# Kernel tuning notes

Hardware: AMD Instinct MI355X
Metric: run time of the kernel (lower is better)

The kernel has to match this reference:

```python
import jax, jax.numpy as jnp
import numpy as np
import math

H = 12
D_MODEL = 768
D_K = D_MODEL // H


def setup_inputs() -> dict:
    key = jax.random.key(0)
    ks = jax.random.split(key, 12)
    B, L = 128, 512
    s = 1.0 / math.sqrt(D_MODEL)
    return {
        "Q": jax.random.normal(ks[0], (B, L, D_MODEL), jnp.float32),
        "K": jax.random.normal(ks[1], (B, L, D_MODEL), jnp.float32),
        "V": jax.random.normal(ks[2], (B, L, D_MODEL), jnp.float32),
        "mask": jax.random.uniform(ks[3], (B, B), jnp.float32),
        "Wq": jax.random.normal(ks[4], (D_MODEL, D_MODEL), jnp.float32) * s,
        "bq": jnp.zeros((D_MODEL,), jnp.float32),
        "Wk": jax.random.normal(ks[5], (D_MODEL, D_MODEL), jnp.float32) * s,
        "bk": jnp.zeros((D_MODEL,), jnp.float32),
        "Wv": jax.random.normal(ks[6], (D_MODEL, D_MODEL), jnp.float32) * s,
        "bv": jnp.zeros((D_MODEL,), jnp.float32),
        "Wo": jax.random.normal(ks[7], (D_MODEL, D_MODEL), jnp.float32) * s,
        "bo": jnp.zeros((D_MODEL,), jnp.float32),
    }


def reference(Q, K, V, mask, Wq, bq, Wk, bk, Wv, bv, Wo, bo):
    nb_q = Q.shape[0]   # nbatches_q = Q.size(0) in the torch code
    nb_kv = K.shape[0]
    # Linear projections then the module's exact reshape/transpose pattern.
    q = (Q @ Wq + bq).reshape(-1, nb_q, H, D_K).swapaxes(1, 2)   # (L, h, B, d_k)
    k = (K @ Wk + bk).reshape(-1, nb_kv, H, D_K).swapaxes(1, 2)  # (L, h, B, d_k)
    v = (V @ Wv + bv).reshape(-1, nb_kv, H, D_K).swapaxes(1, 2)  # (L, h, B, d_k)
    # AttentionAgger: model_dim = d_k -> scale by sqrt(d_k)
    attn = jnp.einsum('lhbd,lhed->lhbe', q, k) / math.sqrt(D_K)  # (L, h, B, B)
    # dual softmax with additive mask bias (mask scaled by its leading dim)
    m = jax.nn.softmax(mask / mask.shape[0], axis=-1)            # (B, B), broadcasts
    attn = jax.nn.softmax(attn, axis=-1) + m
    attn = jax.nn.softmax(attn, axis=-1)
    x = jnp.einsum('lhbe,lhed->lhbd', attn, v)                   # (L, h, B, d_k)
    x = x.swapaxes(1, 2).reshape(-1, nb_q, H * D_K)              # (L, B, d_model)
    return x @ Wo + bo
```

## Files before the change

kernel.cpp:

```cpp
#include <hip/hip_runtime.h>


typedef __attribute__((ext_vector_type(8))) __bf16 bf16x8;
typedef __attribute__((ext_vector_type(4))) __bf16 bf16x4;
typedef __attribute__((ext_vector_type(4))) float f32x4;

#define DM 768
#define LOG2E 1.44269504f

__device__ __forceinline__ unsigned short f2bf(float x) {
  unsigned u = __float_as_uint(x);
  u += 0x7FFFu + ((u >> 16) & 1u);
  return (unsigned short)(u >> 16);
}

__device__ __forceinline__ void gl_lds16(const void* g, void* l) {
  __builtin_amdgcn_global_load_lds(
      (const __attribute__((address_space(1))) unsigned int*)g,
      (__attribute__((address_space(3))) unsigned int*)l, 16, 0, 0);
}

__global__ __launch_bounds__(256) void prep_w(const float* __restrict__ w0,
                                              const float* __restrict__ w1,
                                              const float* __restrict__ w2,
                                              const float* __restrict__ w3,
                                              unsigned short* __restrict__ wt) {
  __shared__ float t[32][33];
  const int op = blockIdx.z;
  const float* w = (op == 0) ? w0 : (op == 1) ? w1 : (op == 2) ? w2 : w3;
  unsigned short* o = wt + (size_t)op * DM * DM;
  const int n0 = blockIdx.x * 32, k0 = blockIdx.y * 32;
  const int tx = threadIdx.x & 31, ty = threadIdx.x >> 5;
#pragma unroll
  for (int r = 0; r < 4; ++r)
    t[r * 8 + ty][tx] = w[(size_t)(k0 + r * 8 + ty) * DM + n0 + tx];
  __syncthreads();
#pragma unroll
  for (int r = 0; r < 4; ++r)
    o[(size_t)(n0 + r * 8 + ty) * DM + k0 + tx] = f2bf(t[tx][r * 8 + ty]);
}

__global__ void prep_m(const float* __restrict__ mask, float* __restrict__ mm) {
  int row = blockIdx.x;
  int t = threadIdx.x;
  float a = mask[row * 128 + t] * (1.0f / 128.0f);
  float b = mask[row * 128 + t + 64] * (1.0f / 128.0f);
  float mx = fmaxf(a, b);
  for (int s = 1; s < 64; s <<= 1) mx = fmaxf(mx, __shfl_xor(mx, s));
  float ea = __expf(a - mx), eb = __expf(b - mx);
  float sum = ea + eb;
  for (int s = 1; s < 64; s <<= 1) sum += __shfl_xor(sum, s);
  float inv = LOG2E / sum;
  mm[row * 128 + t] = ea * inv;
  mm[row * 128 + t + 64] = eb * inv;
}

__global__ __launch_bounds__(256) void convb(const float* __restrict__ in,
                                             unsigned short* __restrict__ out, int n8) {
  int i = blockIdx.x * 256 + threadIdx.x;
  const int stride = gridDim.x * 256;
  for (; i < n8; i += stride) {
    const float4 a = ((const float4*)in)[(size_t)i * 2];
    const float4 b = ((const float4*)in)[(size_t)i * 2 + 1];
    ushort4 lo = {f2bf(a.x), f2bf(a.y), f2bf(a.z), f2bf(a.w)};
    ushort4 hi = {f2bf(b.x), f2bf(b.y), f2bf(b.z), f2bf(b.w)};
    ((ushort4*)out)[(size_t)i * 2] = lo;
    ((ushort4*)out)[(size_t)i * 2 + 1] = hi;
  }
}

__device__ __forceinline__ void stage_tile(const unsigned short* __restrict__ src,
                                           int row0, int kcol, char* slotbase, int tid) {
  const int wid = tid >> 6, lane = tid & 63;
#pragma unroll
  for (int s = 0; s < 2; ++s) {
    const int row = s * 128 + wid * 16 + (lane >> 2);
    const int slot = lane & 3;
    gl_lds16(src + (size_t)(row0 + row) * DM + kcol + ((slot ^ ((row >> 1) & 3)) * 8),
             slotbase + s * 8192 + wid * 1024);
  }
}

template <bool OUT_BF16>
__global__ __launch_bounds__(512, 2) void gemm8(const unsigned short* __restrict__ A,
                                                const unsigned short* __restrict__ Bt,
                                                const float* __restrict__ bias,
                                                void* __restrict__ Outp) {
  __shared__ char smem[131072];
  const int tid = threadIdx.x, lane = tid & 63, wid = tid >> 6;
  const int cl = lane & 15, g = lane >> 4;
  const int wm = wid >> 2, wn = wid & 3;
  const int bid = blockIdx.x;
  const int xcd = bid & 7, bi = bid >> 3;
  const int m0 = (xcd * 32 + bi / 3) * 256;
  const int n0 = (bi % 3) * 256;

  f32x4 acc[8][4] = {};

  auto aslot = [&](int t) { return (char*)smem + (t & 3) * 16384; };
  auto bslot = [&](int t) { return (char*)smem + 65536 + (t & 3) * 16384; };

  auto lda = [&](bf16x8* af, int t, int half) {
#pragma unroll
    for (int mi = 0; mi < 4; ++mi) {
      const int r = wm * 128 + (half * 4 + mi) * 16 + cl;
      af[mi] = *(const bf16x8*)(aslot(t) + r * 64 + ((g ^ ((r >> 1) & 3)) * 16));
    }
  };
  auto ldb = [&](bf16x8* bf, int t) {
#pragma unroll
    for (int ni = 0; ni < 4; ++ni) {
      const int r = wn * 64 + ni * 16 + cl;
      bf[ni] = *(const bf16x8*)(bslot(t) + r * 64 + ((g ^ ((r >> 1) & 3)) * 16));
    }
  };
  auto mfma16 = [&](bf16x8* af, bf16x8* bf, int half) {
    __builtin_amdgcn_s_setprio(1);
#pragma unroll
    for (int mi = 0; mi < 4; ++mi)
#pragma unroll
      for (int ni = 0; ni < 4; ++ni)
        acc[half * 4 + mi][ni] = __builtin_amdgcn_mfma_f32_16x16x32_bf16(
            af[mi], bf[ni], acc[half * 4 + mi][ni], 0, 0, 0);
    __builtin_amdgcn_s_setprio(0);
  };

  auto gstep = [&](int t, bool stg, int vm, bf16x8* af0, bf16x8* bfc,
                   bf16x8* af0n, bf16x8* bfn, bool last) {
    bf16x8 af1[4];
    if (stg) stage_tile(A, m0, (t + 3) * 32, aslot(t + 3), tid);
    if (vm == 6)      asm volatile("s_waitcnt vmcnt(6)" ::: "memory");
    else if (vm == 4) asm volatile("s_waitcnt vmcnt(4)" ::: "memory");
    else              asm volatile("s_waitcnt vmcnt(0)" ::: "memory");
    __builtin_amdgcn_s_barrier();
    lda(af1, t, 1);
    mfma16(af0, bfc, 0);
    if (stg) stage_tile(Bt, n0, (t + 3) * 32, bslot(t + 3), tid);
    if (!last) {
      lda(af0n, t + 1, 0);
      ldb(bfn, t + 1);
    }
    mfma16(af1, bfc, 1);
    __builtin_amdgcn_s_barrier();
  };

  stage_tile(A, m0, 0, aslot(0), tid);   stage_tile(Bt, n0, 0, bslot(0), tid);
  stage_tile(A, m0, 32, aslot(1), tid);  stage_tile(Bt, n0, 32, bslot(1), tid);
  stage_tile(A, m0, 64, aslot(2), tid);  stage_tile(Bt, n0, 64, bslot(2), tid);
  asm volatile("s_waitcnt vmcnt(8)" ::: "memory");
  __builtin_amdgcn_s_barrier();

  bf16x8 afA[4], bfA[4], afB[4], bfB[4];
  lda(afA, 0, 0);
  ldb(bfA, 0);

#pragma unroll 1
  for (int t = 0; t < 20; t += 2) {
    gstep(t, true, 6, afA, bfA, afB, bfB, false);
    gstep(t + 1, true, 6, afB, bfB, afA, bfA, false);
  }
  gstep(20, true, 6, afA, bfA, afB, bfB, false);
  gstep(21, false, 4, afB, bfB, afA, bfA, false);
  gstep(22, false, 0, afA, bfA, afB, bfB, false);
  gstep(23, false, 0, afB, bfB, afA, bfA, true);

  float bb[4];
#pragma unroll
  for (int ni = 0; ni < 4; ++ni) bb[ni] = bias[n0 + wn * 64 + ni * 16 + cl];
#pragma unroll
  for (int mi = 0; mi < 8; ++mi) {
    const int row = m0 + wm * 128 + mi * 16 + g * 4;
#pragma unroll
    for (int ni = 0; ni < 4; ++ni) {
      const int col = n0 + wn * 64 + ni * 16 + cl;
#pragma unroll
      for (int e = 0; e < 4; ++e) {
        float v = acc[mi][ni][e] + bb[ni];
        if constexpr (OUT_BF16)
          ((unsigned short*)Outp)[(size_t)(row + e) * DM + col] = f2bf(v);
        else
          ((float*)Outp)[(size_t)(row + e) * DM + col] = v;
      }
    }
  }
}

__global__ __launch_bounds__(512) void attn_k(const unsigned short* __restrict__ qp,
                                              const unsigned short* __restrict__ kp,
                                              const unsigned short* __restrict__ vp,
                                              const float* __restrict__ mm,
                                              unsigned short* __restrict__ xout) {
  __shared__ char smem[32768];
  unsigned short* vt = (unsigned short*)(smem + 16384);

  const int tid = threadIdx.x, lane = tid & 63, wid = tid >> 6;
  const int cl = lane & 15, g = lane >> 4;
  const int h = blockIdx.x, l = blockIdx.y;
  const size_t base = (size_t)l * 128 * DM + h * 64;
  const int q = wid * 16 + cl;

#pragma unroll
  for (int p = 0; p < 2; ++p) {
    const int chunk = p * 8 + wid;
    const int row = chunk * 8 + (lane >> 3);
    const int gi = (lane & 7) ^ (row & 7);
    gl_lds16(kp + base + (size_t)row * DM + gi * 8, smem + chunk * 1024);
  }
  if (tid < 256) {
    const int dc = (tid & 7) * 8;
    const int kq = tid >> 3;
    const int pg = (kq ^ ((tid & 7) << 2));
    int4 r0 = *(const int4*)&vp[base + (size_t)(kq * 4 + 0) * DM + dc];
    int4 r1 = *(const int4*)&vp[base + (size_t)(kq * 4 + 1) * DM + dc];
    int4 r2 = *(const int4*)&vp[base + (size_t)(kq * 4 + 2) * DM + dc];
    int4 r3 = *(const int4*)&vp[base + (size_t)(kq * 4 + 3) * DM + dc];
    const unsigned short* u0 = (const unsigned short*)&r0;
    const unsigned short* u1 = (const unsigned short*)&r1;
    const unsigned short* u2 = (const unsigned short*)&r2;
    const unsigned short* u3 = (const unsigned short*)&r3;
#pragma unroll
    for (int j = 0; j < 8; ++j) {
      ushort4 w = {u0[j], u1[j], u2[j], u3[j]};
      *(ushort4*)&vt[(dc + j) * 128 + pg * 4] = w;
    }
  }
  bf16x8 qf[2];
#pragma unroll
  for (int ksr = 0; ksr < 2; ++ksr)
    qf[ksr] = *(const bf16x8*)&qp[base + (size_t)q * DM + ksr * 32 + g * 8];
  __syncthreads();

  f32x4 sacc[8] = {};
  __builtin_amdgcn_s_setprio(1);
#pragma unroll
  for (int ksr = 0; ksr < 2; ++ksr) {
#pragma unroll
    for (int kf = 0; kf < 8; ++kf) {
      const int row = kf * 16 + cl;
      const int gi = (ksr * 4 + g) ^ (row & 7);
      bf16x8 kfr = *(const bf16x8*)(smem + row * 128 + gi * 16);
      sacc[kf] = __builtin_amdgcn_mfma_f32_16x16x32_bf16(kfr, qf[ksr], sacc[kf], 0, 0, 0);
    }
  }
  __builtin_amdgcn_s_setprio(0);
  __syncthreads();

  bf16x4 pk[8];
  {
    float4 mrow[8];
#pragma unroll
    for (int kf = 0; kf < 8; ++kf)
      mrow[kf] = *(const float4*)&mm[q * 128 + kf * 16 + g * 4];
    float sm = 0.f;
#pragma unroll
    for (int kf = 0; kf < 8; ++kf)
#pragma unroll
      for (int e = 0; e < 4; ++e) {
        float p = exp2f(sacc[kf][e] * (0.125f * LOG2E));
        sacc[kf][e] = p;
        sm += p;
      }
    sm += __shfl_xor(sm, 16); sm += __shfl_xor(sm, 32);
    const float inv2e = LOG2E / sm;
    float s2 = 0.f;
#pragma unroll
    for (int kf = 0; kf < 8; ++kf)
#pragma unroll
      for (int e = 0; e < 4; ++e) {
        float p = exp2f(fmaf(sacc[kf][e], inv2e, ((const float*)&mrow[kf])[e]));
        sacc[kf][e] = p;
        s2 += p;
      }
    s2 += __shfl_xor(s2, 16); s2 += __shfl_xor(s2, 32);
    const float inv2 = 1.0f / s2;
#pragma unroll
    for (int kf = 0; kf < 8; ++kf)
      pk[kf] = {(__bf16)(sacc[kf][0] * inv2), (__bf16)(sacc[kf][1] * inv2),
                (__bf16)(sacc[kf][2] * inv2), (__bf16)(sacc[kf][3] * inv2)};
  }

  f32x4 xacc[4] = {};

#pragma unroll
  for (int kf = 0; kf < 4; ++kf) {
    const int gi = (kf * 4 + g) ^ ((q & 3) << 2);
    *(bf16x4*)(smem + q * 128 + gi * 8) = pk[kf];
  }
  asm volatile("s_waitcnt lgkmcnt(0)" ::: "memory");
  __builtin_amdgcn_sched_barrier(0);
  __builtin_amdgcn_s_setprio(1);
#pragma unroll
  for (int ks2 = 0; ks2 < 2; ++ks2) {
    const int gi = (ks2 * 8 + g * 2) ^ ((q & 3) << 2);
    bf16x8 pa = *(const bf16x8*)(smem + q * 128 + gi * 8);
#pragma unroll
    for (int fc = 0; fc < 4; ++fc) {
      const int d = fc * 16 + cl;
      const int pg = (ks2 * 8 + 2 * g) ^ (((d >> 3) & 7) << 2);
      bf16x8 bv = *(const bf16x8*)&vt[d * 128 + pg * 4];
      xacc[fc] = __builtin_amdgcn_mfma_f32_16x16x32_bf16(pa, bv, xacc[fc], 0, 0, 0);
    }
  }
  __builtin_amdgcn_s_setprio(0);
  asm volatile("s_waitcnt lgkmcnt(0)" ::: "memory");
  __builtin_amdgcn_sched_barrier(0);

#pragma unroll
  for (int kf = 0; kf < 4; ++kf) {
    const int gi = (kf * 4 + g) ^ ((q & 3) << 2);
    *(bf16x4*)(smem + q * 128 + gi * 8) = pk[4 + kf];
  }
  asm volatile("s_waitcnt lgkmcnt(0)" ::: "memory");
  __builtin_amdgcn_sched_barrier(0);
  __builtin_amdgcn_s_setprio(1);
#pragma unroll
  for (int ks2 = 2; ks2 < 4; ++ks2) {
    const int gi = ((ks2 - 2) * 8 + g * 2) ^ ((q & 3) << 2);
    bf16x8 pa = *(const bf16x8*)(smem + q * 128 + gi * 8);
#pragma unroll
    for (int fc = 0; fc < 4; ++fc) {
      const int d = fc * 16 + cl;
      const int pg = (ks2 * 8 + 2 * g) ^ (((d >> 3) & 7) << 2);
      bf16x8 bv = *(const bf16x8*)&vt[d * 128 + pg * 4];
      xacc[fc] = __builtin_amdgcn_mfma_f32_16x16x32_bf16(pa, bv, xacc[fc], 0, 0, 0);
    }
  }
  __builtin_amdgcn_s_setprio(0);

#pragma unroll
  for (int fc = 0; fc < 4; ++fc)
#pragma unroll
    for (int e = 0; e < 4; ++e) {
      const int qr = wid * 16 + g * 4 + e;
      __bf16 b = (__bf16)xacc[fc][e];
      unsigned short u;
      __builtin_memcpy(&u, &b, 2);
      xout[base + (size_t)qr * DM + fc * 16 + cl] = u;
    }
}

extern "C" void kernel_launch(void* const* d_in, const int* in_sizes, int n_in,
                              void* d_out, int out_size, void* d_ws, size_t ws_size,
                              hipStream_t stream) {
  (void)in_sizes; (void)n_in; (void)out_size; (void)ws_size;
  const float* Q = (const float*)d_in[0];
  const float* K = (const float*)d_in[1];
  const float* V = (const float*)d_in[2];
  const float* mask = (const float*)d_in[3];
  const float* Wq = (const float*)d_in[4];
  const float* bq = (const float*)d_in[5];
  const float* Wk = (const float*)d_in[6];
  const float* bk = (const float*)d_in[7];
  const float* Wv = (const float*)d_in[8];
  const float* bv = (const float*)d_in[9];
  const float* Wo = (const float*)d_in[10];
  const float* bo = (const float*)d_in[11];

  const size_t NP = (size_t)65536 * DM;

  unsigned short* qp = (unsigned short*)d_out;
  unsigned short* kp = qp + NP;
  unsigned short* S1 = (unsigned short*)d_ws;
  unsigned short* S2 = S1 + NP;
  unsigned short* wt = S2 + NP;
  float* mm = (float*)(wt + (size_t)4 * DM * DM);

  prep_w<<<dim3(24, 24, 4), 256, 0, stream>>>(Wq, Wk, Wv, Wo, wt);
  prep_m<<<dim3(128), 64, 0, stream>>>(mask, mm);

  const int n8 = (int)(NP / 8);
  dim3 g8(768);

  convb<<<dim3(2048), 256, 0, stream>>>(Q, S1, n8);
  gemm8<true><<<g8, 512, 0, stream>>>(S1, wt + 0 * (size_t)DM * DM, bq, qp);
  convb<<<dim3(2048), 256, 0, stream>>>(K, S1, n8);
  gemm8<true><<<g8, 512, 0, stream>>>(S1, wt + 1 * (size_t)DM * DM, bk, kp);
  convb<<<dim3(2048), 256, 0, stream>>>(V, S2, n8);
  gemm8<true><<<g8, 512, 0, stream>>>(S2, wt + 2 * (size_t)DM * DM, bv, S1);

  attn_k<<<dim3(12, 512), 512, 0, stream>>>(qp, kp, S1, mm, S1);

  gemm8<false><<<g8, 512, 0, stream>>>(S1, wt + 3 * (size_t)DM * DM, bo, (float*)d_out);
}
```

Before: 662.7 us.

## Process four sequence tiles per attention block with double-buffered K/V prefetch

The attention kernel now loops over four consecutive L tiles per block instead of one, so the grid shrinks by a factor of four. K for the next tile goes into a second LDS buffer, while V and Q for the next tile are loaded into registers during the current tile's compute. The mask rows are loaded once per block and reused across tiles. This is meant to hide global-load latency and cut per-block setup cost, but LDS use rises to 80 KB per block, which can lower the number of resident blocks per CU.

```diff
diff --git a/kernel.cpp b/kernel.cpp
--- a/kernel.cpp
+++ b/kernel.cpp
@@ -185,158 +185,184 @@
   }
 }
 
-__global__ __launch_bounds__(512) void attn_k(const unsigned short* __restrict__ qp,
-                                              const unsigned short* __restrict__ kp,
-                                              const unsigned short* __restrict__ vp,
-                                              const float* __restrict__ mm,
-                                              unsigned short* __restrict__ xout) {
-  __shared__ char smem[32768];
-  unsigned short* vt = (unsigned short*)(smem + 16384);
+#define TPB 4
+
+__global__ __launch_bounds__(512, 4) void attn_k(const unsigned short* __restrict__ qp,
+                                                 const unsigned short* __restrict__ kp,
+                                                 const unsigned short* __restrict__ vp,
+                                                 const float* __restrict__ mm,
+                                                 unsigned short* __restrict__ xout) {
+  __shared__ char smem[81920];
+  char* psb = smem + 65536;
 
   const int tid = threadIdx.x, lane = tid & 63, wid = tid >> 6;
   const int cl = lane & 15, g = lane >> 4;
-  const int h = blockIdx.x, l = blockIdx.y;
-  const size_t base = (size_t)l * 128 * DM + h * 64;
+  const int h = blockIdx.x;
+  const int l0 = blockIdx.y * TPB;
   const int q = wid * 16 + cl;
 
-#pragma unroll
-  for (int p = 0; p < 2; ++p) {
-    const int chunk = p * 8 + wid;
-    const int row = chunk * 8 + (lane >> 3);
-    const int gi = (lane & 7) ^ (row & 7);
-    gl_lds16(kp + base + (size_t)row * DM + gi * 8, smem + chunk * 1024);
-  }
-  if (tid < 256) {
-    const int dc = (tid & 7) * 8;
-    const int kq = tid >> 3;
-    const int pg = (kq ^ ((tid & 7) << 2));
-    int4 r0 = *(const int4*)&vp[base + (size_t)(kq * 4 + 0) * DM + dc];
-    int4 r1 = *(const int4*)&vp[base + (size_t)(kq * 4 + 1) * DM + dc];
-    int4 r2 = *(const int4*)&vp[base + (size_t)(kq * 4 + 2) * DM + dc];
-    int4 r3 = *(const int4*)&vp[base + (size_t)(kq * 4 + 3) * DM + dc];
-    const unsigned short* u0 = (const unsigned short*)&r0;
-    const unsigned short* u1 = (const unsigned short*)&r1;
-    const unsigned short* u2 = (const unsigned short*)&r2;
-    const unsigned short* u3 = (const unsigned short*)&r3;
-#pragma unroll
-    for (int j = 0; j < 8; ++j) {
-      ushort4 w = {u0[j], u1[j], u2[j], u3[j]};
-      *(ushort4*)&vt[(dc + j) * 128 + pg * 4] = w;
-    }
-  }
-  bf16x8 qf[2];
-#pragma unroll
-  for (int ksr = 0; ksr < 2; ++ksr)
-    qf[ksr] = *(const bf16x8*)&qp[base + (size_t)q * DM + ksr * 32 + g * 8];
-  __syncthreads();
-
-  f32x4 sacc[8] = {};
-  __builtin_amdgcn_s_setprio(1);
-#pragma unroll
-  for (int ksr = 0; ksr < 2; ++ksr) {
-#pragma unroll
-    for (int kf = 0; kf < 8; ++kf) {
-      const int row = kf * 16 + cl;
-      const int gi = (ksr * 4 + g) ^ (row & 7);
-      bf16x8 kfr = *(const bf16x8*)(smem + row * 128 + gi * 16);
-      sacc[kf] = __builtin_amdgcn_mfma_f32_16x16x32_bf16(kfr, qf[ksr], sacc[kf], 0, 0, 0);
-    }
-  }
-  __builtin_amdgcn_s_setprio(0);
-  __syncthreads();
-
-  bf16x4 pk[8];
-  {
-    float4 mrow[8];
-#pragma unroll
-    for (int kf = 0; kf < 8; ++kf)
-      mrow[kf] = *(const float4*)&mm[q * 128 + kf * 16 + g * 4];
-    float sm = 0.f;
-#pragma unroll
-    for (int kf = 0; kf < 8; ++kf)
+  auto ksb = [&](int t) { return smem + (t & 1) * 16384; };
+  auto vtb = [&](int t) { return (unsigned short*)(smem + 32768 + (t & 1) * 16384); };
+  auto tbase = [&](int t) { return (size_t)(l0 + t) * 128 * DM + h * 64; };
+
+  const bool vw = tid < 256;
+  const int dc = (tid & 7) * 8;
+  const int kq = (tid & 255) >> 3;
+  int4 vr[4];
+
+  auto loadV = [&](size_t base) {
+    if (vw) {
+#pragma unroll
+      for (int r = 0; r < 4; ++r)
+        vr[r] = *(const int4*)&vp[base + (size_t)(kq * 4 + r) * DM + dc];
+    }
+  };
+  auto writeVT = [&](unsigned short* vt) {
+    if (vw) {
+      const int pg = kq ^ ((tid & 7) << 2);
+      const unsigned short* u0 = (const unsigned short*)&vr[0];
+      const unsigned short* u1 = (const unsigned short*)&vr[1];
+      const unsigned short* u2 = (const unsigned short*)&vr[2];
+      const unsigned short* u3 = (const unsigned short*)&vr[3];
+#pragma unroll
+      for (int j = 0; j < 8; ++j) {
+        ushort4 w = {u0[j], u1[j], u2[j], u3[j]};
+        *(ushort4*)&vt[(dc + j) * 128 + pg * 4] = w;
+      }
+    }
+  };
+  auto stageK = [&](size_t base, char* dst) {
+#pragma unroll
+    for (int p = 0; p < 2; ++p) {
+      const int chunk = p * 8 + wid;
+      const int row = chunk * 8 + (lane >> 3);
+      const int gi = (lane & 7) ^ (row & 7);
+      gl_lds16(kp + base + (size_t)row * DM + gi * 8, dst + chunk * 1024);
+    }
+  };
+  auto loadQ = [&](size_t base, bf16x8* qf) {
+#pragma unroll
+    for (int ksr = 0; ksr < 2; ++ksr)
+      qf[ksr] = *(const bf16x8*)&qp[base + (size_t)q * DM + ksr * 32 + g * 8];
+  };
+
+  float4 mrow[8];
+#pragma unroll
+  for (int kf = 0; kf < 8; ++kf)
+    mrow[kf] = *(const float4*)&mm[q * 128 + kf * 16 + g * 4];
+
+  bf16x8 qfA[2], qfB[2];
+  loadV(tbase(0));
+  loadQ(tbase(0), qfA);
+  stageK(tbase(0), ksb(0));
+  asm volatile("s_waitcnt vmcnt(0)" ::: "memory");
+  __builtin_amdgcn_sched_barrier(0);
+
+  auto iter = [&](int t, bool pf, bf16x8* qf, bf16x8* qn) {
+    writeVT(vtb(t));
+    if (pf) { loadV(tbase(t + 1)); loadQ(tbase(t + 1), qn); }
+    asm volatile("s_waitcnt lgkmcnt(0)" ::: "memory");
+    __builtin_amdgcn_sched_barrier(0);
+    __builtin_amdgcn_s_barrier();
+    if (pf) stageK(tbase(t + 1), ksb(t + 1));
+
+    f32x4 sacc[8] = {};
+    __builtin_amdgcn_s_setprio(1);
+#pragma unroll
+    for (int ksr = 0; ksr < 2; ++ksr) {
+#pragma unroll
+      for (int kf = 0; kf < 8; ++kf) {
+        const int row = kf * 16 + cl;
+        const int gi = (ksr * 4 + g) ^ (row & 7);
+        bf16x8 kfr = *(const bf16x8*)(ksb(t) + row * 128 + gi * 16);
+        sacc[kf] =
+            __builtin_amdgcn_mfma_f32_16x16x32_bf16(kfr, qf[ksr], sacc[kf], 0, 0, 0);
+      }
+    }
+    __builtin_amdgcn_s_setprio(0);
+
+    bf16x4 pk[8];
+    {
+      float sm = 0.f;
+#pragma unroll
+      for (int kf = 0; kf < 8; ++kf)
+#pragma unroll
+        for (int e = 0; e < 4; ++e) {
+          float p = exp2f(sacc[kf][e] * (0.125f * LOG2E));
+          sacc[kf][e] = p;
+          sm += p;
+        }
+      sm += __shfl_xor(sm, 16); sm += __shfl_xor(sm, 32);
+      const float inv2e = LOG2E / sm;
+      float s2 = 0.f;
+#pragma unroll
+      for (int kf = 0; kf < 8; ++kf)
+#pragma unroll
+        for (int e = 0; e < 4; ++e) {
+          float p = exp2f(fmaf(sacc[kf][e], inv2e, ((const float*)&mrow[kf])[e]));
+          sacc[kf][e] = p;
+          s2 += p;
+        }
+      s2 += __shfl_xor(s2, 16); s2 += __shfl_xor(s2, 32);
+      const float inv2 = 1.0f / s2;
+#pragma unroll
+      for (int kf = 0; kf < 8; ++kf)
+        pk[kf] = {(__bf16)(sacc[kf][0] * inv2), (__bf16)(sacc[kf][1] * inv2),
+                  (__bf16)(sacc[kf][2] * inv2), (__bf16)(sacc[kf][3] * inv2)};
+    }
+
+    f32x4 xacc[4] = {};
+    unsigned short* vt = vtb(t);
+#pragma unroll
+    for (int half = 0; half < 2; ++half) {
+#pragma unroll
+      for (int kf = 0; kf < 4; ++kf) {
+        const int gi = (kf * 4 + g) ^ ((q & 3) << 2);
+        *(bf16x4*)(psb + q * 128 + gi * 8) = pk[half * 4 + kf];
+      }
+      asm volatile("s_waitcnt lgkmcnt(0)" ::: "memory");
+      __builtin_amdgcn_sched_barrier(0);
+      __builtin_amdgcn_s_setprio(1);
+#pragma unroll
+      for (int k2 = 0; k2 < 2; ++k2) {
+        const int ks2 = half * 2 + k2;
+        const int gi = (k2 * 8 + g * 2) ^ ((q & 3) << 2);
+        bf16x8 pa = *(const bf16x8*)(psb + q * 128 + gi * 8);
+#pragma unroll
+        for (int fc = 0; fc < 4; ++fc) {
+          const int d = fc * 16 + cl;
+          const int pg = (ks2 * 8 + 2 * g) ^ (((d >> 3) & 7) << 2);
+          bf16x8 bv = *(const bf16x8*)&vt[d * 128 + pg * 4];
+          xacc[fc] = __builtin_amdgcn_mfma_f32_16x16x32_bf16(pa, bv, xacc[fc], 0, 0, 0);
+        }
+      }
+      __builtin_amdgcn_s_setprio(0);
+      if (half == 0) {
+        asm volatile("s_waitcnt lgkmcnt(0)" ::: "memory");
+        __builtin_amdgcn_sched_barrier(0);
+      }
+    }
+
+    asm volatile("s_waitcnt vmcnt(0)" ::: "memory");
+    __builtin_amdgcn_sched_barrier(0);
+
+    const size_t base = tbase(t);
+#pragma unroll
+    for (int fc = 0; fc < 4; ++fc)
 #pragma unroll
       for (int e = 0; e < 4; ++e) {
-        float p = exp2f(sacc[kf][e] * (0.125f * LOG2E));
-        sacc[kf][e] = p;
-        sm += p;
-      }
-    sm += __shfl_xor(sm, 16); sm += __shfl_xor(sm, 32);
-    const float inv2e = LOG2E / sm;
-    float s2 = 0.f;
-#pragma unroll
-    for (int kf = 0; kf < 8; ++kf)
-#pragma unroll
-      for (int e = 0; e < 4; ++e) {
-        float p = exp2f(fmaf(sacc[kf][e], inv2e, ((const float*)&mrow[kf])[e]));
-        sacc[kf][e] = p;
-        s2 += p;
-      }
-    s2 += __shfl_xor(s2, 16); s2 += __shfl_xor(s2, 32);
-    const float inv2 = 1.0f / s2;
-#pragma unroll
-    for (int kf = 0; kf < 8; ++kf)
-      pk[kf] = {(__bf16)(sacc[kf][0] * inv2), (__bf16)(sacc[kf][1] * inv2),
-                (__bf16)(sacc[kf][2] * inv2), (__bf16)(sacc[kf][3] * inv2)};
-  }
-
-  f32x4 xacc[4] = {};
-
-#pragma unroll
-  for (int kf = 0; kf < 4; ++kf) {
-    const int gi = (kf * 4 + g) ^ ((q & 3) << 2);
-    *(bf16x4*)(smem + q * 128 + gi * 8) = pk[kf];
-  }
-  asm volatile("s_waitcnt lgkmcnt(0)" ::: "memory");
-  __builtin_amdgcn_sched_barrier(0);
-  __builtin_amdgcn_s_setprio(1);
-#pragma unroll
-  for (int ks2 = 0; ks2 < 2; ++ks2) {
-    const int gi = (ks2 * 8 + g * 2) ^ ((q & 3) << 2);
-    bf16x8 pa = *(const bf16x8*)(smem + q * 128 + gi * 8);
-#pragma unroll
-    for (int fc = 0; fc < 4; ++fc) {
-      const int d = fc * 16 + cl;
-      const int pg = (ks2 * 8 + 2 * g) ^ (((d >> 3) & 7) << 2);
-      bf16x8 bv = *(const bf16x8*)&vt[d * 128 + pg * 4];
-      xacc[fc] = __builtin_amdgcn_mfma_f32_16x16x32_bf16(pa, bv, xacc[fc], 0, 0, 0);
-    }
-  }
-  __builtin_amdgcn_s_setprio(0);
-  asm volatile("s_waitcnt lgkmcnt(0)" ::: "memory");
-  __builtin_amdgcn_sched_barrier(0);
-
-#pragma unroll
-  for (int kf = 0; kf < 4; ++kf) {
-    const int gi = (kf * 4 + g) ^ ((q & 3) << 2);
-    *(bf16x4*)(smem + q * 128 + gi * 8) = pk[4 + kf];
-  }
-  asm volatile("s_waitcnt lgkmcnt(0)" ::: "memory");
-  __builtin_amdgcn_sched_barrier(0);
-  __builtin_amdgcn_s_setprio(1);
-#pragma unroll
-  for (int ks2 = 2; ks2 < 4; ++ks2) {
-    const int gi = ((ks2 - 2) * 8 + g * 2) ^ ((q & 3) << 2);
-    bf16x8 pa = *(const bf16x8*)(smem + q * 128 + gi * 8);
-#pragma unroll
-    for (int fc = 0; fc < 4; ++fc) {
-      const int d = fc * 16 + cl;
-      const int pg = (ks2 * 8 + 2 * g) ^ (((d >> 3) & 7) << 2);
-      bf16x8 bv = *(const bf16x8*)&vt[d * 128 + pg * 4];
-      xacc[fc] = __builtin_amdgcn_mfma_f32_16x16x32_bf16(pa, bv, xacc[fc], 0, 0, 0);
-    }
-  }
-  __builtin_amdgcn_s_setprio(0);
-
-#pragma unroll
-  for (int fc = 0; fc < 4; ++fc)
-#pragma unroll
-    for (int e = 0; e < 4; ++e) {
-      const int qr = wid * 16 + g * 4 + e;
-      __bf16 b = (__bf16)xacc[fc][e];
-      unsigned short u;
-      __builtin_memcpy(&u, &b, 2);
-      xout[base + (size_t)qr * DM + fc * 16 + cl] = u;
-    }
+        const int qr = wid * 16 + g * 4 + e;
+        __bf16 b = (__bf16)xacc[fc][e];
+        unsigned short u;
+        __builtin_memcpy(&u, &b, 2);
+        xout[base + (size_t)qr * DM + fc * 16 + cl] = u;
+      }
+  };
+
+  iter(0, true, qfA, qfB);
+  iter(1, true, qfB, qfA);
+  iter(2, true, qfA, qfB);
+  iter(3, false, qfB, qfA);
 }
 
 extern "C" void kernel_launch(void* const* d_in, const int* in_sizes, int n_in,
@@ -378,7 +404,7 @@
   convb<<<dim3(2048), 256, 0, stream>>>(V, S2, n8);
   gemm8<true><<<g8, 512, 0, stream>>>(S2, wt + 2 * (size_t)DM * DM, bv, S1);
 
-  attn_k<<<dim3(12, 512), 512, 0, stream>>>(qp, kp, S1, mm, S1);
+  attn_k<<<dim3(12, 128), 512, 0, stream>>>(qp, kp, S1, mm, S1);
 
   gemm8<false><<<g8, 512, 0, stream>>>(S1, wt + 3 * (size_t)DM * DM, bo, (float*)d_out);
 }
```

Measured after the change: 760.0 us. 1.15x slower.

## Fuse fp32-to-bf16 input conversion into projection GEMM A-tile loading

Applied to the files above, without the earlier changes.

Removes the separate convb kernels that converted Q, K and V to bf16 in workspace. The projection GEMM now loads fp32 A rows into registers, converts them to bf16 and writes them into the swizzled LDS slots one pipeline step ahead, with waitcnt counts adjusted to match. This drops a full read-write round trip of three large activation tensors. In exchange the GEMM reads twice as many A bytes, uses more registers for staging, and adds LDS writes plus an lgkmcnt wait inside each step. The attention PV loop is also folded into a loop over halves, which is only cosmetic.

```diff
diff --git a/kernel.cpp b/kernel.cpp
--- a/kernel.cpp
+++ b/kernel.cpp
@@ -18,6 +18,17 @@
   __builtin_amdgcn_global_load_lds(
       (const __attribute__((address_space(1))) unsigned int*)g,
       (__attribute__((address_space(3))) unsigned int*)l, 16, 0, 0);
+}
+
+__device__ __forceinline__ void waitvm(int n) {
+  switch (n) {
+    case 0:  asm volatile("s_waitcnt vmcnt(0)" ::: "memory"); break;
+    case 2:  asm volatile("s_waitcnt vmcnt(2)" ::: "memory"); break;
+    case 4:  asm volatile("s_waitcnt vmcnt(4)" ::: "memory"); break;
+    case 6:  asm volatile("s_waitcnt vmcnt(6)" ::: "memory"); break;
+    case 8:  asm volatile("s_waitcnt vmcnt(8)" ::: "memory"); break;
+    default: asm volatile("s_waitcnt vmcnt(10)" ::: "memory"); break;
+  }
 }
 
 __global__ __launch_bounds__(256) void prep_w(const float* __restrict__ w0,
@@ -55,20 +66,6 @@
   mm[row * 128 + t + 64] = eb * inv;
 }
 
-__global__ __launch_bounds__(256) void convb(const float* __restrict__ in,
-                                             unsigned short* __restrict__ out, int n8) {
-  int i = blockIdx.x * 256 + threadIdx.x;
-  const int stride = gridDim.x * 256;
-  for (; i < n8; i += stride) {
-    const float4 a = ((const float4*)in)[(size_t)i * 2];
-    const float4 b = ((const float4*)in)[(size_t)i * 2 + 1];
-    ushort4 lo = {f2bf(a.x), f2bf(a.y), f2bf(a.z), f2bf(a.w)};
-    ushort4 hi = {f2bf(b.x), f2bf(b.y), f2bf(b.z), f2bf(b.w)};
-    ((ushort4*)out)[(size_t)i * 2] = lo;
-    ((ushort4*)out)[(size_t)i * 2 + 1] = hi;
-  }
-}
-
 __device__ __forceinline__ void stage_tile(const unsigned short* __restrict__ src,
                                            int row0, int kcol, char* slotbase, int tid) {
   const int wid = tid >> 6, lane = tid & 63;
@@ -81,12 +78,14 @@
   }
 }
 
-template <bool OUT_BF16>
-__global__ __launch_bounds__(512, 2) void gemm8(const unsigned short* __restrict__ A,
+template <bool OUT_BF16, bool A_FP32>
+__global__ __launch_bounds__(512, 2) void gemm8(const void* __restrict__ Ap,
                                                 const unsigned short* __restrict__ Bt,
                                                 const float* __restrict__ bias,
                                                 void* __restrict__ Outp) {
   __shared__ char smem[131072];
+  const unsigned short* A16 = (const unsigned short*)Ap;
+  const float* A32 = (const float*)Ap;
   const int tid = threadIdx.x, lane = tid & 63, wid = tid >> 6;
   const int cl = lane & 15, g = lane >> 4;
   const int wm = wid >> 2, wn = wid & 3;
@@ -100,6 +99,28 @@
   auto aslot = [&](int t) { return (char*)smem + (t & 3) * 16384; };
   auto bslot = [&](int t) { return (char*)smem + 65536 + (t & 3) * 16384; };
 
+  const int arow = tid >> 1, ahalf = tid & 1;
+  float4 ar0[4], ar1[4];
+  auto aloadR = [&](int t, float4* buf) {
+    const float* src = &A32[(size_t)(m0 + arow) * DM + t * 32 + ahalf * 16];
+#pragma unroll
+    for (int i = 0; i < 4; ++i) buf[i] = *(const float4*)(src + i * 4);
+  };
+  auto awrite = [&](int t, const float4* buf) {
+    const float* f = (const float*)buf;
+    bf16x8 v0, v1;
+#pragma unroll
+    for (int j = 0; j < 8; ++j) {
+      v0[j] = (__bf16)f[j];
+      v1[j] = (__bf16)f[8 + j];
+    }
+    const int m = (arow >> 1) & 3;
+    const int s0 = (ahalf * 2) ^ m;
+    char* base = aslot(t) + arow * 64;
+    *(bf16x8*)(base + s0 * 16) = v0;
+    *(bf16x8*)(base + (s0 ^ 1) * 16) = v1;
+  };
+
   auto lda = [&](bf16x8* af, int t, int half) {
 #pragma unroll
     for (int mi = 0; mi < 4; ++mi) {
@@ -125,13 +146,15 @@
     __builtin_amdgcn_s_setprio(0);
   };
 
-  auto gstep = [&](int t, bool stg, int vm, bf16x8* af0, bf16x8* bfc,
-                   bf16x8* af0n, bf16x8* bfn, bool last) {
+  auto gstep = [&](int t, bool stg, int vm, bool wr, float4* arL, float4* arW,
+                   bf16x8* af0, bf16x8* bfc, bf16x8* af0n, bf16x8* bfn, bool last) {
     bf16x8 af1[4];
-    if (stg) stage_tile(A, m0, (t + 3) * 32, aslot(t + 3), tid);
-    if (vm == 6)      asm volatile("s_waitcnt vmcnt(6)" ::: "memory");
-    else if (vm == 4) asm volatile("s_waitcnt vmcnt(4)" ::: "memory");
-    else              asm volatile("s_waitcnt vmcnt(0)" ::: "memory");
+    if constexpr (A_FP32) {
+      if (stg) aloadR(t + 3, arL);
+    } else {
+      if (stg) stage_tile(A16, m0, (t + 3) * 32, aslot(t + 3), tid);
+    }
+    waitvm(vm);
     __builtin_amdgcn_s_barrier();
     lda(af1, t, 1);
     mfma16(af0, bfc, 0);
@@ -141,28 +164,59 @@
       ldb(bfn, t + 1);
     }
     mfma16(af1, bfc, 1);
+    if constexpr (A_FP32) {
+      if (wr) {
+        awrite(t + 2, arW);
+        asm volatile("s_waitcnt lgkmcnt(0)" ::: "memory");
+        __builtin_amdgcn_sched_barrier(0);
+      }
+    }
     __builtin_amdgcn_s_barrier();
   };
 
-  stage_tile(A, m0, 0, aslot(0), tid);   stage_tile(Bt, n0, 0, bslot(0), tid);
-  stage_tile(A, m0, 32, aslot(1), tid);  stage_tile(Bt, n0, 32, bslot(1), tid);
-  stage_tile(A, m0, 64, aslot(2), tid);  stage_tile(Bt, n0, 64, bslot(2), tid);
-  asm volatile("s_waitcnt vmcnt(8)" ::: "memory");
-  __builtin_amdgcn_s_barrier();
+  if constexpr (A_FP32) {
+    aloadR(0, ar0);
+    stage_tile(Bt, n0, 0, bslot(0), tid);
+    aloadR(1, ar1);
+    stage_tile(Bt, n0, 32, bslot(1), tid);
+    waitvm(8);
+    awrite(0, ar0);
+    aloadR(2, ar0);
+    waitvm(6);
+    awrite(1, ar1);
+    stage_tile(Bt, n0, 64, bslot(2), tid);
+    asm volatile("s_waitcnt lgkmcnt(0)" ::: "memory");
+    __builtin_amdgcn_sched_barrier(0);
+    __builtin_amdgcn_s_barrier();
+  } else {
+    stage_tile(A16, m0, 0, aslot(0), tid);  stage_tile(Bt, n0, 0, bslot(0), tid);
+    stage_tile(A16, m0, 32, aslot(1), tid); stage_tile(Bt, n0, 32, bslot(1), tid);
+    stage_tile(A16, m0, 64, aslot(2), tid); stage_tile(Bt, n0, 64, bslot(2), tid);
+    asm volatile("s_waitcnt vmcnt(8)" ::: "memory");
+    __builtin_amdgcn_s_barrier();
+  }
 
   bf16x8 afA[4], bfA[4], afB[4], bfB[4];
   lda(afA, 0, 0);
   ldb(bfA, 0);
 
+  constexpr int VMs = A_FP32 ? 10 : 6;
 #pragma unroll 1
   for (int t = 0; t < 20; t += 2) {
-    gstep(t, true, 6, afA, bfA, afB, bfB, false);
-    gstep(t + 1, true, 6, afB, bfB, afA, bfA, false);
-  }
-  gstep(20, true, 6, afA, bfA, afB, bfB, false);
-  gstep(21, false, 4, afB, bfB, afA, bfA, false);
-  gstep(22, false, 0, afA, bfA, afB, bfB, false);
-  gstep(23, false, 0, afB, bfB, afA, bfA, true);
+    gstep(t, true, VMs, true, ar1, ar0, afA, bfA, afB, bfB, false);
+    gstep(t + 1, true, VMs, true, ar0, ar1, afB, bfB, afA, bfA, false);
+  }
+  if constexpr (A_FP32) {
+    gstep(20, true, 10, true, ar1, ar0, afA, bfA, afB, bfB, false);
+    gstep(21, false, 6, true, ar0, ar1, afB, bfB, afA, bfA, false);
+    gstep(22, false, 0, false, ar1, ar0, afA, bfA, afB, bfB, false);
+    gstep(23, false, 0, false, ar0, ar1, afB, bfB, afA, bfA, true);
+  } else {
+    gstep(20, true, 6, false, ar1, ar0, afA, bfA, afB, bfB, false);
+    gstep(21, false, 4, false, ar0, ar1, afB, bfB, afA, bfA, false);
+    gstep(22, false, 0, false, ar1, ar0, afA, bfA, afB, bfB, false);
+    gstep(23, false, 0, false, ar0, ar1, afB, bfB, afA, bfA, true);
+  }
 
   float bb[4];
 #pragma unroll
@@ -280,52 +334,35 @@
   }
 
   f32x4 xacc[4] = {};
-
-#pragma unroll
-  for (int kf = 0; kf < 4; ++kf) {
-    const int gi = (kf * 4 + g) ^ ((q & 3) << 2);
-    *(bf16x4*)(smem + q * 128 + gi * 8) = pk[kf];
-  }
-  asm volatile("s_waitcnt lgkmcnt(0)" ::: "memory");
-  __builtin_amdgcn_sched_barrier(0);
-  __builtin_amdgcn_s_setprio(1);
-#pragma unroll
-  for (int ks2 = 0; ks2 < 2; ++ks2) {
-    const int gi = (ks2 * 8 + g * 2) ^ ((q & 3) << 2);
-    bf16x8 pa = *(const bf16x8*)(smem + q * 128 + gi * 8);
-#pragma unroll
-    for (int fc = 0; fc < 4; ++fc) {
-      const int d = fc * 16 + cl;
-      const int pg = (ks2 * 8 + 2 * g) ^ (((d >> 3) & 7) << 2);
-      bf16x8 bv = *(const bf16x8*)&vt[d * 128 + pg * 4];
-      xacc[fc] = __builtin_amdgcn_mfma_f32_16x16x32_bf16(pa, bv, xacc[fc], 0, 0, 0);
-    }
-  }
-  __builtin_amdgcn_s_setprio(0);
-  asm volatile("s_waitcnt lgkmcnt(0)" ::: "memory");
-  __builtin_amdgcn_sched_barrier(0);
-
-#pragma unroll
-  for (int kf = 0; kf < 4; ++kf) {
-    const int gi = (kf * 4 + g) ^ ((q & 3) << 2);
-    *(bf16x4*)(smem + q * 128 + gi * 8) = pk[4 + kf];
-  }
-  asm volatile("s_waitcnt lgkmcnt(0)" ::: "memory");
-  __builtin_amdgcn_sched_barrier(0);
-  __builtin_amdgcn_s_setprio(1);
-#pragma unroll
-  for (int ks2 = 2; ks2 < 4; ++ks2) {
-    const int gi = ((ks2 - 2) * 8 + g * 2) ^ ((q & 3) << 2);
-    bf16x8 pa = *(const bf16x8*)(smem + q * 128 + gi * 8);
-#pragma unroll
-    for (int fc = 0; fc < 4; ++fc) {
-      const int d = fc * 16 + cl;
-      const int pg = (ks2 * 8 + 2 * g) ^ (((d >> 3) & 7) << 2);
-      bf16x8 bv = *(const bf16x8*)&vt[d * 128 + pg * 4];
-      xacc[fc] = __builtin_amdgcn_mfma_f32_16x16x32_bf16(pa, bv, xacc[fc], 0, 0, 0);
-    }
-  }
-  __builtin_amdgcn_s_setprio(0);
+#pragma unroll
+  for (int half = 0; half < 2; ++half) {
+#pragma unroll
+    for (int kf = 0; kf < 4; ++kf) {
+      const int gi = (kf * 4 + g) ^ ((q & 3) << 2);
+      *(bf16x4*)(smem + q * 128 + gi * 8) = pk[half * 4 + kf];
+    }
+    asm volatile("s_waitcnt lgkmcnt(0)" ::: "memory");
+    __builtin_amdgcn_sched_barrier(0);
+    __builtin_amdgcn_s_setprio(1);
+#pragma unroll
+    for (int k2 = 0; k2 < 2; ++k2) {
+      const int ks2 = half * 2 + k2;
+      const int gi = (k2 * 8 + g * 2) ^ ((q & 3) << 2);
+      bf16x8 pa = *(const bf16x8*)(smem + q * 128 + gi * 8);
+#pragma unroll
+      for (int fc = 0; fc < 4; ++fc) {
+        const int d = fc * 16 + cl;
+        const int pg = (ks2 * 8 + 2 * g) ^ (((d >> 3) & 7) << 2);
+        bf16x8 bv = *(const bf16x8*)&vt[d * 128 + pg * 4];
+        xacc[fc] = __builtin_amdgcn_mfma_f32_16x16x32_bf16(pa, bv, xacc[fc], 0, 0, 0);
+      }
+    }
+    __builtin_amdgcn_s_setprio(0);
+    if (half == 0) {
+      asm volatile("s_waitcnt lgkmcnt(0)" ::: "memory");
+      __builtin_amdgcn_sched_barrier(0);
+    }
+  }
 
 #pragma unroll
   for (int fc = 0; fc < 4; ++fc)
@@ -361,24 +398,20 @@
   unsigned short* qp = (unsigned short*)d_out;
   unsigned short* kp = qp + NP;
   unsigned short* S1 = (unsigned short*)d_ws;
-  unsigned short* S2 = S1 + NP;
-  unsigned short* wt = S2 + NP;
+  unsigned short* wt = S1 + NP;
   float* mm = (float*)(wt + (size_t)4 * DM * DM);
 
   prep_w<<<dim3(24, 24, 4), 256, 0, stream>>>(Wq, Wk, Wv, Wo, wt);
   prep_m<<<dim3(128), 64, 0, stream>>>(mask, mm);
 
-  const int n8 = (int)(NP / 8);
   dim3 g8(768);
 
-  convb<<<dim3(2048), 256, 0, stream>>>(Q, S1, n8);
-  gemm8<true><<<g8, 512, 0, stream>>>(S1, wt + 0 * (size_t)DM * DM, bq, qp);
-  convb<<<dim3(2048), 256, 0, stream>>>(K, S1, n8);
-  gemm8<true><<<g8, 512, 0, stream>>>(S1, wt + 1 * (size_t)DM * DM, bk, kp);
-  convb<<<dim3(2048), 256, 0, stream>>>(V, S2, n8);
-  gemm8<true><<<g8, 512, 0, stream>>>(S2, wt + 2 * (size_t)DM * DM, bv, S1);
+  gemm8<true, true><<<g8, 512, 0, stream>>>(Q, wt + 0 * (size_t)DM * DM, bq, qp);
+  gemm8<true, true><<<g8, 512, 0, stream>>>(K, wt + 1 * (size_t)DM * DM, bk, kp);
+  gemm8<true, true><<<g8, 512, 0, stream>>>(V, wt + 2 * (size_t)DM * DM, bv, S1);
 
   attn_k<<<dim3(12, 512), 512, 0, stream>>>(qp, kp, S1, mm, S1);
 
-  gemm8<false><<<g8, 512, 0, stream>>>(S1, wt + 3 * (size_t)DM * DM, bo, (float*)d_out);
-}
+  gemm8<false, false><<<g8, 512, 0, stream>>>(S1, wt + 3 * (size_t)DM * DM, bo,
+                                              (float*)d_out);
+}
```

Measured after the change: 752.1 us. 13.5% more time.

## Restructure GEMM pipeline to stage two K-tiles per barrier round

Applied to the files above, without the earlier changes.

Replaces the GEMM main loop's three-deep, one-tile-per-step software pipeline, which preloaded register fragments across barriers, with a loop that stages two K-tiles per iteration. Each iteration waits, hits one barrier pair, then loads and consumes both tiles from LDS. This halves the number of barrier rounds, but LDS fragment loads are no longer overlapped with MFMAs from the previous step, and prefetch depth drops to one iteration ahead. The attention PV section is also folded into a loop over two halves, which produces the same code and is a cleanup.

```diff
diff --git a/kernel.cpp b/kernel.cpp
--- a/kernel.cpp
+++ b/kernel.cpp
@@ -125,44 +125,37 @@
     __builtin_amdgcn_s_setprio(0);
   };
 
-  auto gstep = [&](int t, bool stg, int vm, bf16x8* af0, bf16x8* bfc,
-                   bf16x8* af0n, bf16x8* bfn, bool last) {
-    bf16x8 af1[4];
-    if (stg) stage_tile(A, m0, (t + 3) * 32, aslot(t + 3), tid);
-    if (vm == 6)      asm volatile("s_waitcnt vmcnt(6)" ::: "memory");
-    else if (vm == 4) asm volatile("s_waitcnt vmcnt(4)" ::: "memory");
-    else              asm volatile("s_waitcnt vmcnt(0)" ::: "memory");
+  auto stg2 = [&](int u) {
+    stage_tile(A, m0, u * 32, aslot(u), tid);
+    stage_tile(Bt, n0, u * 32, bslot(u), tid);
+  };
+
+  stg2(0); stg2(1);
+  asm volatile("s_waitcnt vmcnt(0)" ::: "memory");
+  __builtin_amdgcn_s_barrier();
+
+  bf16x8 afA[4], af1[4], afB[4], bfA[4], bfB[4];
+
+#pragma unroll 1
+  for (int t = 0; t < 12; ++t) {
+    const int u = 2 * t;
+    if (t < 11) {
+      stg2(u + 2); stg2(u + 3);
+      asm volatile("s_waitcnt vmcnt(8)" ::: "memory");
+    } else {
+      asm volatile("s_waitcnt vmcnt(0)" ::: "memory");
+    }
     __builtin_amdgcn_s_barrier();
-    lda(af1, t, 1);
-    mfma16(af0, bfc, 0);
-    if (stg) stage_tile(Bt, n0, (t + 3) * 32, bslot(t + 3), tid);
-    if (!last) {
-      lda(af0n, t + 1, 0);
-      ldb(bfn, t + 1);
-    }
-    mfma16(af1, bfc, 1);
+    lda(afA, u, 0); ldb(bfA, u);
+    lda(af1, u, 1);
+    mfma16(afA, bfA, 0);
+    lda(afB, u + 1, 0); ldb(bfB, u + 1);
+    mfma16(af1, bfA, 1);
+    lda(afA, u + 1, 1);
+    mfma16(afB, bfB, 0);
+    mfma16(afA, bfB, 1);
     __builtin_amdgcn_s_barrier();
-  };
-
-  stage_tile(A, m0, 0, aslot(0), tid);   stage_tile(Bt, n0, 0, bslot(0), tid);
-  stage_tile(A, m0, 32, aslot(1), tid);  stage_tile(Bt, n0, 32, bslot(1), tid);
-  stage_tile(A, m0, 64, aslot(2), tid);  stage_tile(Bt, n0, 64, bslot(2), tid);
-  asm volatile("s_waitcnt vmcnt(8)" ::: "memory");
-  __builtin_amdgcn_s_barrier();
-
-  bf16x8 afA[4], bfA[4], afB[4], bfB[4];
-  lda(afA, 0, 0);
-  ldb(bfA, 0);
-
-#pragma unroll 1
-  for (int t = 0; t < 20; t += 2) {
-    gstep(t, true, 6, afA, bfA, afB, bfB, false);
-    gstep(t + 1, true, 6, afB, bfB, afA, bfA, false);
-  }
-  gstep(20, true, 6, afA, bfA, afB, bfB, false);
-  gstep(21, false, 4, afB, bfB, afA, bfA, false);
-  gstep(22, false, 0, afA, bfA, afB, bfB, false);
-  gstep(23, false, 0, afB, bfB, afA, bfA, true);
+  }
 
   float bb[4];
 #pragma unroll
@@ -280,52 +273,35 @@
   }
 
   f32x4 xacc[4] = {};
-
-#pragma unroll
-  for (int kf = 0; kf < 4; ++kf) {
-    const int gi = (kf * 4 + g) ^ ((q & 3) << 2);
-    *(bf16x4*)(smem + q * 128 + gi * 8) = pk[kf];
-  }
-  asm volatile("s_waitcnt lgkmcnt(0)" ::: "memory");
-  __builtin_amdgcn_sched_barrier(0);
-  __builtin_amdgcn_s_setprio(1);
-#pragma unroll
-  for (int ks2 = 0; ks2 < 2; ++ks2) {
-    const int gi = (ks2 * 8 + g * 2) ^ ((q & 3) << 2);
-    bf16x8 pa = *(const bf16x8*)(smem + q * 128 + gi * 8);
-#pragma unroll
-    for (int fc = 0; fc < 4; ++fc) {
-      const int d = fc * 16 + cl;
-      const int pg = (ks2 * 8 + 2 * g) ^ (((d >> 3) & 7) << 2);
-      bf16x8 bv = *(const bf16x8*)&vt[d * 128 + pg * 4];
-      xacc[fc] = __builtin_amdgcn_mfma_f32_16x16x32_bf16(pa, bv, xacc[fc], 0, 0, 0);
-    }
-  }
-  __builtin_amdgcn_s_setprio(0);
-  asm volatile("s_waitcnt lgkmcnt(0)" ::: "memory");
-  __builtin_amdgcn_sched_barrier(0);
-
-#pragma unroll
-  for (int kf = 0; kf < 4; ++kf) {
-    const int gi = (kf * 4 + g) ^ ((q & 3) << 2);
-    *(bf16x4*)(smem + q * 128 + gi * 8) = pk[4 + kf];
-  }
-  asm volatile("s_waitcnt lgkmcnt(0)" ::: "memory");
-  __builtin_amdgcn_sched_barrier(0);
-  __builtin_amdgcn_s_setprio(1);
-#pragma unroll
-  for (int ks2 = 2; ks2 < 4; ++ks2) {
-    const int gi = ((ks2 - 2) * 8 + g * 2) ^ ((q & 3) << 2);
-    bf16x8 pa = *(const bf16x8*)(smem + q * 128 + gi * 8);
-#pragma unroll
-    for (int fc = 0; fc < 4; ++fc) {
-      const int d = fc * 16 + cl;
-      const int pg = (ks2 * 8 + 2 * g) ^ (((d >> 3) & 7) << 2);
-      bf16x8 bv = *(const bf16x8*)&vt[d * 128 + pg * 4];
-      xacc[fc] = __builtin_amdgcn_mfma_f32_16x16x32_bf16(pa, bv, xacc[fc], 0, 0, 0);
-    }
-  }
-  __builtin_amdgcn_s_setprio(0);
+#pragma unroll
+  for (int half = 0; half < 2; ++half) {
+#pragma unroll
+    for (int kf = 0; kf < 4; ++kf) {
+      const int gi = (kf * 4 + g) ^ ((q & 3) << 2);
+      *(bf16x4*)(smem + q * 128 + gi * 8) = pk[half * 4 + kf];
+    }
+    asm volatile("s_waitcnt lgkmcnt(0)" ::: "memory");
+    __builtin_amdgcn_sched_barrier(0);
+    __builtin_amdgcn_s_setprio(1);
+#pragma unroll
+    for (int k2 = 0; k2 < 2; ++k2) {
+      const int ks2 = half * 2 + k2;
+      const int gi = (k2 * 8 + g * 2) ^ ((q & 3) << 2);
+      bf16x8 pa = *(const bf16x8*)(smem + q * 128 + gi * 8);
+#pragma unroll
+      for (int fc = 0; fc < 4; ++fc) {
+        const int d = fc * 16 + cl;
+        const int pg = (ks2 * 8 + 2 * g) ^ (((d >> 3) & 7) << 2);
+        bf16x8 bv = *(const bf16x8*)&vt[d * 128 + pg * 4];
+        xacc[fc] = __builtin_amdgcn_mfma_f32_16x16x32_bf16(pa, bv, xacc[fc], 0, 0, 0);
+      }
+    }
+    __builtin_amdgcn_s_setprio(0);
+    if (half == 0) {
+      asm volatile("s_waitcnt lgkmcnt(0)" ::: "memory");
+      __builtin_amdgcn_sched_barrier(0);
+    }
+  }
 
 #pragma unroll
   for (int fc = 0; fc < 4; ++fc)
```

Result: slower. 734.4 us (+10.8%).
